# Performance work log

Measured on AMD Instinct MI355X. Metric: run time of the kernel, lower is better.

## Reference

```python
import jax, jax.numpy as jnp
import numpy as np

B, N, D = 2, 1024, 1024
H = 4
KD = 512          # key_dim = d_model * 0.5
VD = 1024         # value_dim = d_model
DK = KD // H      # 128 head_qk_dim
DV = VD // H      # 256 head_v_dim
LR = 16           # gate_low_rank_dim
GLN = 16.0        # gate_logit_normalizer
EPS = 1e-5


def setup_inputs() -> dict:
    key = jax.random.key(0)
    ks = jax.random.split(key, 10)
    s = 0.02
    return {
        "x": jax.random.normal(ks[0], (B, N, D), jnp.float32),
        "Wq": jax.random.normal(ks[1], (D, KD), jnp.float32) * s,
        "Wk": jax.random.normal(ks[2], (D, KD), jnp.float32) * s,
        "Wv": jax.random.normal(ks[3], (D, VD), jnp.float32) * s,
        "Wg": jax.random.normal(ks[4], (D, VD), jnp.float32) * s,
        "Wgk1": jax.random.normal(ks[5], (D, LR), jnp.float32) * s,
        "Wgk2": jax.random.normal(ks[6], (LR, KD), jnp.float32) * s,
        "bgk2": jax.random.normal(ks[7], (KD,), jnp.float32) * s,
        "Wout": jax.random.normal(ks[8], (VD, D), jnp.float32) * s,
        "rms_w": jnp.ones((DV,), jnp.float32),
    }


def _split_heads(t, h):
    b, n, hd = t.shape
    return t.reshape(b, n, h, hd // h).transpose(0, 2, 1, 3)  # b h n d


def _gla_scan(q, k, v, g):
    # q,k: [b,h,n,dk]; v: [b,h,n,dv]; g: [b,h,n,dk] (log-decay)
    b, h, n, dk = q.shape
    dv = v.shape[-1]
    qT = jnp.moveaxis(q, 2, 0)  # [n,b,h,dk]
    kT = jnp.moveaxis(k, 2, 0)
    vT = jnp.moveaxis(v, 2, 0)
    gT = jnp.moveaxis(g, 2, 0)

    def step(S, inp):
        qt, kt, vt, gt = inp
        # S_t = diag(exp(g_t)) S_{t-1} + k_t v_t^T ; o_t = q_t S_t
        S = S * jnp.exp(gt)[..., None] + kt[..., None] * vt[..., None, :]
        ot = jnp.einsum('bhk,bhkv->bhv', qt, S)
        return S, ot

    S0 = jnp.zeros((b, h, dk, dv), q.dtype)
    _, o = jax.lax.scan(step, S0, (qT, kT, vT, gT))
    return jnp.moveaxis(o, 0, 2)  # [b,h,n,dv]


def reference(x, Wq, Wk, Wv, Wg, Wgk1, Wgk2, bgk2, Wout, rms_w):
    q = _split_heads(x @ Wq, H)
    k = _split_heads(x @ Wk, H)
    v = _split_heads(x @ Wv, H)
    g = jax.nn.log_sigmoid((x @ Wgk1) @ Wgk2 + bgk2) / GLN
    g = jnp.maximum(g, -3.0)  # chunk mode clamp
    g = _split_heads(g, H)
    o = _gla_scan(q, k, v, g)               # [b,h,n,dv]
    o = o.transpose(0, 2, 1, 3)             # [b,n,h,dv]
    # RMSNorm over head_v_dim
    o = o * jax.lax.rsqrt(jnp.mean(o * o, axis=-1, keepdims=True) + EPS) * rms_w
    o = o.reshape(o.shape[0], o.shape[1], VD)
    o = o * jax.nn.silu(x @ Wg)
    return o @ Wout
```

## Files before the change

### kernel.cpp

```cpp
#include <hip/hip_runtime.h>
#include <math.h>


typedef __attribute__((ext_vector_type(4))) float vf4;
typedef __attribute__((ext_vector_type(4))) unsigned int vu4;
typedef __attribute__((ext_vector_type(8))) short short8;

#define DEVI static __device__ __forceinline__
DEVI vf4 vzero() { vf4 x = {0.f, 0.f, 0.f, 0.f}; return x; }

DEVI float bf2f(unsigned int u) {
  union { unsigned int i; float f; } c; c.i = u << 16; return c.f;
}
DEVI unsigned short f2bf(float f) {
  union { float f; unsigned int i; } c; c.f = f;
  unsigned int i = c.i;
  return (unsigned short)((i + 0x7fffu + ((i >> 16) & 1u)) >> 16);
}
DEVI void unpack8(vu4 r, float* f) {
  f[0] = bf2f(r.x & 0xffffu); f[1] = bf2f(r.x >> 16);
  f[2] = bf2f(r.y & 0xffffu); f[3] = bf2f(r.y >> 16);
  f[4] = bf2f(r.z & 0xffffu); f[5] = bf2f(r.z >> 16);
  f[6] = bf2f(r.w & 0xffffu); f[7] = bf2f(r.w >> 16);
}
DEVI void unpack16(const unsigned short* p, float* f) {
  unpack8(*(const vu4*)p, f);
  unpack8(*(const vu4*)(p + 8), f + 8);
}
DEVI vu4 pack8(const float* f) {
  vu4 o;
  o.x = (unsigned int)f2bf(f[0]) | ((unsigned int)f2bf(f[1]) << 16);
  o.y = (unsigned int)f2bf(f[2]) | ((unsigned int)f2bf(f[3]) << 16);
  o.z = (unsigned int)f2bf(f[4]) | ((unsigned int)f2bf(f[5]) << 16);
  o.w = (unsigned int)f2bf(f[6]) | ((unsigned int)f2bf(f[7]) << 16);
  return o;
}

__global__ __launch_bounds__(256)
void prep_k(const float* __restrict__ Wq, const float* __restrict__ Wk,
            const float* __restrict__ Wv, const float* __restrict__ Wg,
            const float* __restrict__ Wo, const float* __restrict__ X,
            unsigned short* __restrict__ wqT, unsigned short* __restrict__ wkT,
            unsigned short* __restrict__ wvT, unsigned short* __restrict__ wgT,
            unsigned short* __restrict__ woT, unsigned short* __restrict__ xb) {
  __shared__ float T[64][65];
  const int ct = blockIdx.x, kt = blockIdx.y;
  const int t = threadIdx.x;
  const int r = t >> 2, s = t & 3;
  if (ct >= 64) {
    const int rt = ct - 64;
    const size_t base = (size_t)(rt * 64 + r) * 1024 + kt * 64 + s * 16;
    float f[16];
    *(vf4*)&f[0]  = *(const vf4*)(X + base);
    *(vf4*)&f[4]  = *(const vf4*)(X + base + 4);
    *(vf4*)&f[8]  = *(const vf4*)(X + base + 8);
    *(vf4*)&f[12] = *(const vf4*)(X + base + 12);
    *(vu4*)(xb + base) = pack8(f);
    *(vu4*)(xb + base + 8) = pack8(f + 8);
    return;
  }
  const float* W; unsigned short* O; int N; int cb;
  if (ct < 8)       { W = Wq; O = wqT; N = 512;  cb = ct; }
  else if (ct < 16) { W = Wk; O = wkT; N = 512;  cb = ct - 8; }
  else if (ct < 32) { W = Wv; O = wvT; N = 1024; cb = ct - 16; }
  else if (ct < 48) { W = Wg; O = wgT; N = 1024; cb = ct - 32; }
  else              { W = Wo; O = woT; N = 1024; cb = ct - 48; }
  const float* src = W + (size_t)(kt * 64 + r) * N + cb * 64 + s * 16;
#pragma unroll
  for (int u = 0; u < 4; ++u) {
    vf4 v4 = *(const vf4*)(src + u * 4);
    T[r][s * 16 + u * 4 + 0] = v4.x;
    T[r][s * 16 + u * 4 + 1] = v4.y;
    T[r][s * 16 + u * 4 + 2] = v4.z;
    T[r][s * 16 + u * 4 + 3] = v4.w;
  }
  __syncthreads();
  unsigned int pk[8];
#pragma unroll
  for (int u = 0; u < 8; ++u) {
    unsigned int lo = f2bf(T[s * 16 + 2 * u][r]);
    unsigned int hi = f2bf(T[s * 16 + 2 * u + 1][r]);
    pk[u] = lo | (hi << 16);
  }
  unsigned short* dst = O + (size_t)(cb * 64 + r) * 1024 + kt * 64 + s * 16;
  *(vu4*)dst = *(vu4*)&pk[0];
  *(vu4*)(dst + 8) = *(vu4*)&pk[4];
}

__global__ __launch_bounds__(256)
void proj_mfma_k(const unsigned short* __restrict__ xb,
                 const unsigned short* __restrict__ wqT, const unsigned short* __restrict__ wkT,
                 const unsigned short* __restrict__ wvT, const unsigned short* __restrict__ wgT,
                 unsigned short* __restrict__ qb, unsigned short* __restrict__ kb,
                 unsigned short* __restrict__ vb, unsigned short* __restrict__ sgb) {
  __shared__ __align__(16) unsigned short As[128 * 72];
  __shared__ __align__(16) unsigned short Bs[128 * 72];
  const int t = threadIdx.x;
  const int m0 = blockIdx.y << 7;
  const int nt = blockIdx.x;
  const unsigned short* WT; int n0; int kind;
  if (nt < 4)       { WT = wqT; n0 = nt * 128;        kind = 0; }
  else if (nt < 8)  { WT = wkT; n0 = (nt - 4) * 128;  kind = 1; }
  else if (nt < 16) { WT = wvT; n0 = (nt - 8) * 128;  kind = 2; }
  else              { WT = wgT; n0 = (nt - 16) * 128; kind = 3; }

  const int w = t >> 6, lane = t & 63;
  const int wm = (w >> 1) * 64, wn = (w & 1) * 64;
  const int qd = lane >> 4, m = lane & 15;

  vf4 acc[4][4];
#pragma unroll
  for (int i = 0; i < 4; ++i)
#pragma unroll
    for (int j = 0; j < 4; ++j) acc[i][j] = vzero();

  for (int k0 = 0; k0 < 1024; k0 += 64) {
    __syncthreads();
#pragma unroll
    for (int u2 = 0; u2 < 4; ++u2) {
      const int id = t + (u2 << 8);
      const int row = id >> 3, kg = id & 7;
      vu4 ra = *(const vu4*)(xb + (size_t)(m0 + row) * 1024 + k0 + kg * 8);
      *(vu4*)&As[row * 72 + kg * 8] = ra;
      vu4 rb = *(const vu4*)(WT + (size_t)(n0 + row) * 1024 + k0 + kg * 8);
      *(vu4*)&Bs[row * 72 + kg * 8] = rb;
    }
    __syncthreads();
#pragma unroll
    for (int ks = 0; ks < 2; ++ks) {
      short8 af[4], bf[4];
#pragma unroll
      for (int i = 0; i < 4; ++i) {
        af[i] = *(const short8*)&As[(wm + i * 16 + m) * 72 + ks * 32 + qd * 8];
        bf[i] = *(const short8*)&Bs[(wn + i * 16 + m) * 72 + ks * 32 + qd * 8];
      }
#pragma unroll
      for (int i = 0; i < 4; ++i)
#pragma unroll
        for (int j = 0; j < 4; ++j)
          acc[i][j] = __builtin_amdgcn_mfma_f32_16x16x32_bf16(af[i], bf[j], acc[i][j], 0, 0, 0);
    }
  }
#pragma unroll
  for (int i = 0; i < 4; ++i) {
#pragma unroll
    for (int j = 0; j < 4; ++j) {
#pragma unroll
      for (int r = 0; r < 4; ++r) {
        const int grow = m0 + wm + i * 16 + qd * 4 + r;
        const int gcol = n0 + wn + j * 16 + m;
        float val = acc[i][j][r];
        if (kind == 0)      qb[(size_t)grow * 512 + gcol] = f2bf(val);
        else if (kind == 1) kb[(size_t)grow * 512 + gcol] = f2bf(val);
        else if (kind == 2) vb[(size_t)grow * 1024 + gcol] = f2bf(val);
        else {
          val = val / (1.f + expf(-val));
          sgb[(size_t)grow * 1024 + gcol] = f2bf(val);
        }
      }
    }
  }
}

__global__ __launch_bounds__(256)
void out_mfma_k(const unsigned short* __restrict__ Ab,
                const unsigned short* __restrict__ woT, float* __restrict__ Y) {
  __shared__ __align__(16) unsigned short As[128 * 72];
  __shared__ __align__(16) unsigned short Bs[128 * 72];
  const int t = threadIdx.x;
  const int m0 = blockIdx.y << 7;
  const int n0 = blockIdx.x << 7;
  const int w = t >> 6, lane = t & 63;
  const int wm = (w >> 1) * 64, wn = (w & 1) * 64;
  const int qd = lane >> 4, m = lane & 15;

  vf4 acc[4][4];
#pragma unroll
  for (int i = 0; i < 4; ++i)
#pragma unroll
    for (int j = 0; j < 4; ++j) acc[i][j] = vzero();

  for (int k0 = 0; k0 < 1024; k0 += 64) {
    __syncthreads();
#pragma unroll
    for (int u2 = 0; u2 < 4; ++u2) {
      const int id = t + (u2 << 8);
      const int row = id >> 3, kg = id & 7;
      vu4 ra = *(const vu4*)(Ab + (size_t)(m0 + row) * 1024 + k0 + kg * 8);
      *(vu4*)&As[row * 72 + kg * 8] = ra;
      vu4 rb = *(const vu4*)(woT + (size_t)(n0 + row) * 1024 + k0 + kg * 8);
      *(vu4*)&Bs[row * 72 + kg * 8] = rb;
    }
    __syncthreads();
#pragma unroll
    for (int ks = 0; ks < 2; ++ks) {
      short8 af[4], bf[4];
#pragma unroll
      for (int i = 0; i < 4; ++i) {
        af[i] = *(const short8*)&As[(wm + i * 16 + m) * 72 + ks * 32 + qd * 8];
        bf[i] = *(const short8*)&Bs[(wn + i * 16 + m) * 72 + ks * 32 + qd * 8];
      }
#pragma unroll
      for (int i = 0; i < 4; ++i)
#pragma unroll
        for (int j = 0; j < 4; ++j)
          acc[i][j] = __builtin_amdgcn_mfma_f32_16x16x32_bf16(af[i], bf[j], acc[i][j], 0, 0, 0);
    }
  }
#pragma unroll
  for (int i = 0; i < 4; ++i)
#pragma unroll
    for (int j = 0; j < 4; ++j)
#pragma unroll
      for (int r = 0; r < 4; ++r) {
        const int grow = m0 + wm + i * 16 + qd * 4 + r;
        const int gcol = n0 + wn + j * 16 + m;
        Y[(size_t)grow * 1024 + gcol] = acc[i][j][r];
      }
}

__global__ __launch_bounds__(64)
void lowrank_k(const float* __restrict__ X, const float* __restrict__ W1,
               float* __restrict__ xl) {
  const int row = blockIdx.x;
  const int t = threadIdx.x;
  float acc[16];
#pragma unroll
  for (int c2 = 0; c2 < 16; ++c2) acc[c2] = 0.f;
  const float* xp = X + (size_t)row * 1024 + t * 16;
  float xv[16];
#pragma unroll
  for (int u = 0; u < 4; ++u)
    *(vf4*)&xv[u * 4] = *(const vf4*)(xp + u * 4);
#pragma unroll
  for (int j = 0; j < 16; ++j) {
    const float* wp = W1 + (size_t)(t * 16 + j) * 16;
    float wv[16];
#pragma unroll
    for (int u = 0; u < 4; ++u)
      *(vf4*)&wv[u * 4] = *(const vf4*)(wp + u * 4);
#pragma unroll
    for (int c2 = 0; c2 < 16; ++c2) acc[c2] = fmaf(xv[j], wv[c2], acc[c2]);
  }
#pragma unroll
  for (int mm = 1; mm < 64; mm <<= 1) {
#pragma unroll
    for (int c2 = 0; c2 < 16; ++c2) acc[c2] += __shfl_xor(acc[c2], mm, 64);
  }
  if (t == 0) {
#pragma unroll
    for (int c2 = 0; c2 < 16; ++c2) xl[(size_t)row * 16 + c2] = acc[c2];
  }
}

__global__ __launch_bounds__(256)
void gate_scan_k(const float* __restrict__ xl, const float* __restrict__ W2,
                 const float* __restrict__ bias,
                 unsigned short* __restrict__ q, unsigned short* __restrict__ k,
                 float* __restrict__ ebtot) {
  const int t = threadIdx.x;
  const int w = t >> 6, lane = t & 63;
  const int wid = blockIdx.x * 4 + w;
  const int kcol = wid & 511;
  const int c = (wid >> 9) & 15;
  const int b = wid >> 13;
  const size_t rowbase = (size_t)b * 1024 + c * 64;

  const float* xp = xl + (rowbase + lane) * 16;
  float xv[16];
#pragma unroll
  for (int u = 0; u < 4; ++u)
    *(vf4*)&xv[u * 4] = *(const vf4*)(xp + u * 4);
  float z = bias[kcol];
#pragma unroll
  for (int r = 0; r < 16; ++r) z = fmaf(xv[r], W2[r * 512 + kcol], z);
  float ls = fminf(z, 0.f) - log1pf(expf(-fabsf(z)));
  float g = fmaxf(ls * (1.f / 16.f), -3.f);

#pragma unroll
  for (int d = 1; d < 64; d <<= 1) {
    float up = __shfl_up(g, d, 64);
    if (lane >= d) g += up;
  }

  const size_t a = (rowbase + lane) * 512 + kcol;
  float qv = bf2f((unsigned int)q[a]) * expf(g);
  float kv = bf2f((unsigned int)k[a]) * expf(fminf(-g, 80.f));
  q[a] = f2bf(qv);
  k[a] = f2bf(kv);
  if (lane == 63)
    ebtot[((size_t)b * 16 + c) * 512 + kcol] = expf(g);
}

__global__ __launch_bounds__(256)
void intra_k(const unsigned short* __restrict__ q16, const unsigned short* __restrict__ k16,
             const unsigned short* __restrict__ v, float* __restrict__ o) {
  __shared__ __align__(16) unsigned short Qs[64 * 136];
  __shared__ __align__(16) unsigned short Ks[64 * 136];
  __shared__ float As[64 * 68];
  __shared__ float Vs[64 * 64];
  const int t = threadIdx.x;
  const int vh = blockIdx.x, c = blockIdx.y, bh = blockIdx.z;
  const int b = bh >> 2, h = bh & 3;
  const size_t rowbase = (size_t)b * 1024 + c * 64;

#pragma unroll
  for (int u2 = 0; u2 < 4; ++u2) {
    const int id = t + (u2 << 8);
    const int row = id >> 4, kg = id & 15;
    *(vu4*)&Qs[row * 136 + kg * 8] =
        *(const vu4*)(q16 + (rowbase + row) * 512 + h * 128 + kg * 8);
    *(vu4*)&Ks[row * 136 + kg * 8] =
        *(const vu4*)(k16 + (rowbase + row) * 512 + h * 128 + kg * 8);
  }
  __syncthreads();

  {
    const int w = t >> 6, lane = t & 63;
    const int qd = lane >> 4, m = lane & 15;
    short8 af[4];
#pragma unroll
    for (int kf = 0; kf < 4; ++kf)
      af[kf] = *(const short8*)&Qs[(w * 16 + m) * 136 + kf * 32 + qd * 8];
    vf4 acc[4];
#pragma unroll
    for (int jt = 0; jt < 4; ++jt) acc[jt] = vzero();
#pragma unroll
    for (int jt = 0; jt < 4; ++jt)
#pragma unroll
      for (int kf = 0; kf < 4; ++kf) {
        short8 bfr = *(const short8*)&Ks[(jt * 16 + m) * 136 + kf * 32 + qd * 8];
        acc[jt] = __builtin_amdgcn_mfma_f32_16x16x32_bf16(af[kf], bfr, acc[jt], 0, 0, 0);
      }
#pragma unroll
    for (int jt = 0; jt < 4; ++jt)
#pragma unroll
      for (int r = 0; r < 4; ++r) {
        const int i = w * 16 + qd * 4 + r;
        const int j = jt * 16 + m;
        As[i * 68 + j] = (j <= i) ? acc[jt][r] : 0.f;
      }
  }

  const int i2 = t >> 2, sb = t & 3;
  for (int p = 0; p < 2; ++p) {
    const int vt = vh * 2 + p;
    __syncthreads();
    {
      const int r = t >> 2, s = t & 3;
      const unsigned short* vp = v + (rowbase + r) * 1024 + h * 256 + vt * 64 + s * 16;
      float f[16];
      unpack16(vp, f);
#pragma unroll
      for (int u = 0; u < 16; ++u) Vs[r * 64 + s * 16 + u] = f[u];
    }
    __syncthreads();
    vf4 acc[4];
#pragma unroll
    for (int u = 0; u < 4; ++u) acc[u] = vzero();
    for (int jj = 0; jj < 64; ++jj) {
      const float a = As[i2 * 68 + jj];
#pragma unroll
      for (int u = 0; u < 4; ++u)
        acc[u] += a * *(const vf4*)&Vs[jj * 64 + sb * 16 + u * 4];
    }
    float* op = o + (rowbase + i2) * 1024 + h * 256 + vt * 64 + sb * 16;
#pragma unroll
    for (int u = 0; u < 4; ++u) *(vf4*)(op + u * 4) = acc[u];
  }
}

__global__ __launch_bounds__(256)
void kv_k(const unsigned short* __restrict__ k16, const unsigned short* __restrict__ v,
          unsigned short* __restrict__ ST) {
  __shared__ float Ks[64 * 128];
  __shared__ float Vs[64 * 64];
  const int t = threadIdx.x;
  const int vt = blockIdx.x, c = blockIdx.y, bh = blockIdx.z;
  const int b = bh >> 2, h = bh & 3;
  const size_t rowbase = (size_t)b * 1024 + c * 64;
  {
    const int r = t >> 2, s = t & 3;
    const unsigned short* kp = k16 + (rowbase + r) * 512 + h * 128 + s * 32;
    float fk[32];
    unpack16(kp, fk);
    unpack16(kp + 16, fk + 16);
#pragma unroll
    for (int u = 0; u < 8; ++u)
      *(vf4*)&Ks[r * 128 + s * 32 + u * 4] = *(const vf4*)&fk[u * 4];
    const unsigned short* vp = v + (rowbase + r) * 1024 + h * 256 + vt * 64 + s * 16;
    float f[16];
    unpack16(vp, f);
#pragma unroll
    for (int u = 0; u < 16; ++u) Vs[r * 64 + s * 16 + u] = f[u];
  }
  __syncthreads();
  const int kk = t >> 1, half = t & 1;
  float su[32];
#pragma unroll
  for (int u = 0; u < 32; ++u) su[u] = 0.f;
  for (int j = 0; j < 64; ++j) {
    const float kv = Ks[j * 128 + kk];
    const float* vrow = &Vs[j * 64 + half * 32];
#pragma unroll
    for (int u = 0; u < 32; ++u) su[u] = fmaf(kv, vrow[u], su[u]);
  }
  unsigned short* Sp = ST + ((size_t)(bh * 16 + c) * 256 + vt * 64 + half * 32) * 128 + kk;
#pragma unroll
  for (int u = 0; u < 32; ++u)
    Sp[(size_t)u * 128] = f2bf(su[u]);
}

__global__ __launch_bounds__(256)
void state_scan_k(unsigned short* __restrict__ ST, const float* __restrict__ ebtot) {
  const int idx = blockIdx.x * 256 + threadIdx.x;
  const int kg = idx & 15;
  const int vv = (idx >> 4) & 255;
  const int bh = idx >> 12;
  const int b = bh >> 2, h = bh & 3;
  float s[8];
#pragma unroll
  for (int u = 0; u < 8; ++u) s[u] = 0.f;
  for (int c = 0; c < 16; ++c) {
    unsigned short* p = ST + ((size_t)(bh * 16 + c) * 256 + vv) * 128 + kg * 8;
    const float* ep = ebtot + ((size_t)b * 16 + c) * 512 + h * 128 + kg * 8;
    float e[8];
    *(vf4*)&e[0] = *(const vf4*)ep;
    *(vf4*)&e[4] = *(const vf4*)(ep + 4);
    float kv[8];
    unpack8(*(const vu4*)p, kv);
    *(vu4*)p = pack8(s);
#pragma unroll
    for (int u = 0; u < 8; ++u) s[u] = (s[u] + kv[u]) * e[u];
  }
}

__global__ __launch_bounds__(256)
void o_inter_k(const unsigned short* __restrict__ q16, const unsigned short* __restrict__ ST,
               float* __restrict__ o) {
  __shared__ __align__(16) unsigned short Qs[64 * 136];
  __shared__ __align__(16) unsigned short Ss[128 * 136];
  const int t = threadIdx.x;
  const int vt = blockIdx.x, c = blockIdx.y, bh = blockIdx.z;
  const int b = bh >> 2, h = bh & 3;
  const size_t rowbase = (size_t)b * 1024 + c * 64;

#pragma unroll
  for (int u2 = 0; u2 < 4; ++u2) {
    const int id = t + (u2 << 8);
    const int row = id >> 4, kg = id & 15;
    *(vu4*)&Qs[row * 136 + kg * 8] =
        *(const vu4*)(q16 + (rowbase + row) * 512 + h * 128 + kg * 8);
  }
#pragma unroll
  for (int u2 = 0; u2 < 8; ++u2) {
    const int id = t + (u2 << 8);
    const int vrow = id >> 4, kg = id & 15;
    *(vu4*)&Ss[vrow * 136 + kg * 8] =
        *(const vu4*)(ST + ((size_t)(bh * 16 + c) * 256 + vt * 128 + vrow) * 128 + kg * 8);
  }
  __syncthreads();

  const int w = t >> 6, lane = t & 63;
  const int qd = lane >> 4, m = lane & 15;
  short8 af[4];
#pragma unroll
  for (int kf = 0; kf < 4; ++kf)
    af[kf] = *(const short8*)&Qs[(w * 16 + m) * 136 + kf * 32 + qd * 8];
#pragma unroll
  for (int nt = 0; nt < 8; ++nt) {
    vf4 acc = vzero();
#pragma unroll
    for (int kf = 0; kf < 4; ++kf) {
      short8 bfr = *(const short8*)&Ss[(nt * 16 + m) * 136 + kf * 32 + qd * 8];
      acc = __builtin_amdgcn_mfma_f32_16x16x32_bf16(af[kf], bfr, acc, 0, 0, 0);
    }
    float* base = o + (rowbase + w * 16 + qd * 4) * 1024 + h * 256 + vt * 128 + nt * 16 + m;
#pragma unroll
    for (int r = 0; r < 4; ++r)
      base[(size_t)r * 1024] += acc[r];
  }
}

__global__ __launch_bounds__(256)
void norm_gate_k(const float* __restrict__ o, const float* __restrict__ rmsw,
                 const unsigned short* __restrict__ sg,
                 unsigned short* __restrict__ ob) {
  __shared__ float red[4];
  const int grp = blockIdx.x;
  const int row = grp >> 2, h = grp & 3;
  const int t = threadIdx.x;
  const size_t idx = (size_t)row * 1024 + h * 256 + t;
  const float val = o[idx];
  float ss = val * val;
#pragma unroll
  for (int mm = 1; mm < 64; mm <<= 1) ss += __shfl_xor(ss, mm, 64);
  if ((t & 63) == 0) red[t >> 6] = ss;
  __syncthreads();
  const float tot = red[0] + red[1] + red[2] + red[3];
  const float scale = rsqrtf(tot * (1.f / 256.f) + 1e-5f);
  ob[idx] = f2bf(val * scale * rmsw[t] * bf2f((unsigned int)sg[idx]));
}

extern "C" void kernel_launch(void* const* d_in, const int* in_sizes, int n_in,
                              void* d_out, int out_size, void* d_ws, size_t ws_size,
                              hipStream_t stream) {
  const float* x    = (const float*)d_in[0];
  const float* Wq   = (const float*)d_in[1];
  const float* Wk   = (const float*)d_in[2];
  const float* Wv   = (const float*)d_in[3];
  const float* Wg   = (const float*)d_in[4];
  const float* Wgk1 = (const float*)d_in[5];
  const float* Wgk2 = (const float*)d_in[6];
  const float* bgk2 = (const float*)d_in[7];
  const float* Wout = (const float*)d_in[8];
  const float* rmsw = (const float*)d_in[9];

  const size_t MB = 1u << 20;
  char* w = (char*)d_ws;
  unsigned short* qb16   = (unsigned short*)(w);
  unsigned short* kb16   = (unsigned short*)(w + 2 * MB);
  unsigned short* vbuf   = (unsigned short*)(w + 4 * MB);
  unsigned short* sgbuf  = (unsigned short*)(w + 8 * MB);
  float*          obuf   = (float*)(w + 12 * MB);
  char*           sreg   = w + 20 * MB;
  unsigned short* xb     = (unsigned short*)sreg;
  unsigned short* STbuf  = (unsigned short*)sreg;
  unsigned short* obuf_b = (unsigned short*)sreg;
  float*          xlbuf  = (float*)(w + 28 * MB);
  float*          ebbuf  = (float*)(w + 28 * MB + 131072);
  unsigned short* wqT    = (unsigned short*)(w + 29 * MB);
  unsigned short* wkT    = (unsigned short*)(w + 30 * MB);
  unsigned short* wvT    = (unsigned short*)(w + 31 * MB);
  unsigned short* wgT    = (unsigned short*)(w + 33 * MB);
  unsigned short* woT    = (unsigned short*)(w + 35 * MB);

  prep_k<<<dim3(96, 16), 256, 0, stream>>>(Wq, Wk, Wv, Wg, Wout, x,
                                           wqT, wkT, wvT, wgT, woT, xb);
  lowrank_k<<<2048, 64, 0, stream>>>(x, Wgk1, xlbuf);
  proj_mfma_k<<<dim3(24, 16), 256, 0, stream>>>(xb, wqT, wkT, wvT, wgT, qb16, kb16, vbuf, sgbuf);
  gate_scan_k<<<4096, 256, 0, stream>>>(xlbuf, Wgk2, bgk2, qb16, kb16, ebbuf);
  intra_k<<<dim3(2, 16, 8), 256, 0, stream>>>(qb16, kb16, vbuf, obuf);
  kv_k<<<dim3(4, 16, 8), 256, 0, stream>>>(kb16, vbuf, STbuf);
  state_scan_k<<<128, 256, 0, stream>>>(STbuf, ebbuf);
  o_inter_k<<<dim3(2, 16, 8), 256, 0, stream>>>(qb16, STbuf, obuf);
  norm_gate_k<<<8192, 256, 0, stream>>>(obuf, rmsw, sgbuf, obuf_b);
  out_mfma_k<<<dim3(8, 16), 256, 0, stream>>>(obuf_b, woT, (float*)d_out);
}
```

Before: 226.3 us.

## Fuse intra-chunk attention and chunk state computation into one MFMA kernel

Merges the intra-chunk attention kernel and the per-chunk K^T V state kernel into one kernel that loads Q, K and V once into shared memory. Transposed K and V tiles are kept in LDS. Both the A·V product and the K^T V state product now use bf16 MFMA instructions instead of scalar fp32 FMA loops. This removes a kernel launch and the duplicate global loads of K and V. In exchange, the attention matrix A is rounded to bf16 before multiplying V, and the scattered transposed LDS writes may cause bank conflicts.

```diff
diff --git a/kernel.cpp b/kernel.cpp
--- a/kernel.cpp
+++ b/kernel.cpp
@@ -22,10 +22,6 @@
   f[2] = bf2f(r.y & 0xffffu); f[3] = bf2f(r.y >> 16);
   f[4] = bf2f(r.z & 0xffffu); f[5] = bf2f(r.z >> 16);
   f[6] = bf2f(r.w & 0xffffu); f[7] = bf2f(r.w >> 16);
-}
-DEVI void unpack16(const unsigned short* p, float* f) {
-  unpack8(*(const vu4*)p, f);
-  unpack8(*(const vu4*)(p + 8), f + 8);
 }
 DEVI vu4 pack8(const float* f) {
   vu4 o;
@@ -293,12 +289,14 @@
 }
 
 __global__ __launch_bounds__(256)
-void intra_k(const unsigned short* __restrict__ q16, const unsigned short* __restrict__ k16,
-             const unsigned short* __restrict__ v, float* __restrict__ o) {
+void intra_kv_k(const unsigned short* __restrict__ q16, const unsigned short* __restrict__ k16,
+                const unsigned short* __restrict__ v, float* __restrict__ o,
+                unsigned short* __restrict__ ST) {
   __shared__ __align__(16) unsigned short Qs[64 * 136];
   __shared__ __align__(16) unsigned short Ks[64 * 136];
-  __shared__ float As[64 * 68];
-  __shared__ float Vs[64 * 64];
+  __shared__ __align__(16) unsigned short Kt[128 * 68];
+  __shared__ __align__(16) unsigned short Vt[128 * 68];
+  __shared__ __align__(16) unsigned short Asb[64 * 68];
   const int t = threadIdx.x;
   const int vh = blockIdx.x, c = blockIdx.y, bh = blockIdx.z;
   const int b = bh >> 2, h = bh & 3;
@@ -308,16 +306,26 @@
   for (int u2 = 0; u2 < 4; ++u2) {
     const int id = t + (u2 << 8);
     const int row = id >> 4, kg = id & 15;
-    *(vu4*)&Qs[row * 136 + kg * 8] =
-        *(const vu4*)(q16 + (rowbase + row) * 512 + h * 128 + kg * 8);
-    *(vu4*)&Ks[row * 136 + kg * 8] =
-        *(const vu4*)(k16 + (rowbase + row) * 512 + h * 128 + kg * 8);
+    vu4 rq = *(const vu4*)(q16 + (rowbase + row) * 512 + h * 128 + kg * 8);
+    *(vu4*)&Qs[row * 136 + kg * 8] = rq;
+    vu4 rk = *(const vu4*)(k16 + (rowbase + row) * 512 + h * 128 + kg * 8);
+    *(vu4*)&Ks[row * 136 + kg * 8] = rk;
+    const unsigned short* kp = (const unsigned short*)&rk;
+#pragma unroll
+    for (int u = 0; u < 8; ++u)
+      Kt[(kg * 8 + u) * 68 + row] = kp[u];
+    vu4 rv = *(const vu4*)(v + (rowbase + row) * 1024 + h * 256 + vh * 128 + kg * 8);
+    const unsigned short* vp = (const unsigned short*)&rv;
+#pragma unroll
+    for (int u = 0; u < 8; ++u)
+      Vt[(kg * 8 + u) * 68 + row] = vp[u];
   }
   __syncthreads();
 
+  const int w = t >> 6, lane = t & 63;
+  const int qd = lane >> 4, m = lane & 15;
+
   {
-    const int w = t >> 6, lane = t & 63;
-    const int qd = lane >> 4, m = lane & 15;
     short8 af[4];
 #pragma unroll
     for (int kf = 0; kf < 4; ++kf)
@@ -338,77 +346,62 @@
       for (int r = 0; r < 4; ++r) {
         const int i = w * 16 + qd * 4 + r;
         const int j = jt * 16 + m;
-        As[i * 68 + j] = (j <= i) ? acc[jt][r] : 0.f;
-      }
-  }
-
-  const int i2 = t >> 2, sb = t & 3;
-  for (int p = 0; p < 2; ++p) {
-    const int vt = vh * 2 + p;
-    __syncthreads();
-    {
-      const int r = t >> 2, s = t & 3;
-      const unsigned short* vp = v + (rowbase + r) * 1024 + h * 256 + vt * 64 + s * 16;
-      float f[16];
-      unpack16(vp, f);
-#pragma unroll
-      for (int u = 0; u < 16; ++u) Vs[r * 64 + s * 16 + u] = f[u];
-    }
-    __syncthreads();
-    vf4 acc[4];
-#pragma unroll
-    for (int u = 0; u < 4; ++u) acc[u] = vzero();
-    for (int jj = 0; jj < 64; ++jj) {
-      const float a = As[i2 * 68 + jj];
-#pragma unroll
-      for (int u = 0; u < 4; ++u)
-        acc[u] += a * *(const vf4*)&Vs[jj * 64 + sb * 16 + u * 4];
-    }
-    float* op = o + (rowbase + i2) * 1024 + h * 256 + vt * 64 + sb * 16;
-#pragma unroll
-    for (int u = 0; u < 4; ++u) *(vf4*)(op + u * 4) = acc[u];
-  }
-}
-
-__global__ __launch_bounds__(256)
-void kv_k(const unsigned short* __restrict__ k16, const unsigned short* __restrict__ v,
-          unsigned short* __restrict__ ST) {
-  __shared__ float Ks[64 * 128];
-  __shared__ float Vs[64 * 64];
-  const int t = threadIdx.x;
-  const int vt = blockIdx.x, c = blockIdx.y, bh = blockIdx.z;
-  const int b = bh >> 2, h = bh & 3;
-  const size_t rowbase = (size_t)b * 1024 + c * 64;
+        Asb[i * 68 + j] = f2bf((j <= i) ? acc[jt][r] : 0.f);
+      }
+  }
+  __syncthreads();
+
   {
-    const int r = t >> 2, s = t & 3;
-    const unsigned short* kp = k16 + (rowbase + r) * 512 + h * 128 + s * 32;
-    float fk[32];
-    unpack16(kp, fk);
-    unpack16(kp + 16, fk + 16);
-#pragma unroll
-    for (int u = 0; u < 8; ++u)
-      *(vf4*)&Ks[r * 128 + s * 32 + u * 4] = *(const vf4*)&fk[u * 4];
-    const unsigned short* vp = v + (rowbase + r) * 1024 + h * 256 + vt * 64 + s * 16;
-    float f[16];
-    unpack16(vp, f);
-#pragma unroll
-    for (int u = 0; u < 16; ++u) Vs[r * 64 + s * 16 + u] = f[u];
-  }
-  __syncthreads();
-  const int kk = t >> 1, half = t & 1;
-  float su[32];
-#pragma unroll
-  for (int u = 0; u < 32; ++u) su[u] = 0.f;
-  for (int j = 0; j < 64; ++j) {
-    const float kv = Ks[j * 128 + kk];
-    const float* vrow = &Vs[j * 64 + half * 32];
-#pragma unroll
-    for (int u = 0; u < 32; ++u) su[u] = fmaf(kv, vrow[u], su[u]);
-  }
-  unsigned short* Sp = ST + ((size_t)(bh * 16 + c) * 256 + vt * 64 + half * 32) * 128 + kk;
-#pragma unroll
-  for (int u = 0; u < 32; ++u)
-    Sp[(size_t)u * 128] = f2bf(su[u]);
+    vf4 acc2[4][2];
+#pragma unroll
+    for (int mt = 0; mt < 4; ++mt) { acc2[mt][0] = vzero(); acc2[mt][1] = vzero(); }
+#pragma unroll
+    for (int kf = 0; kf < 2; ++kf) {
+      short8 bf0 = *(const short8*)&Vt[(w * 32 + m) * 68 + kf * 32 + qd * 8];
+      short8 bf1 = *(const short8*)&Vt[(w * 32 + 16 + m) * 68 + kf * 32 + qd * 8];
+#pragma unroll
+      for (int mt = 0; mt < 4; ++mt) {
+        short8 af = *(const short8*)&Asb[(mt * 16 + m) * 68 + kf * 32 + qd * 8];
+        acc2[mt][0] = __builtin_amdgcn_mfma_f32_16x16x32_bf16(af, bf0, acc2[mt][0], 0, 0, 0);
+        acc2[mt][1] = __builtin_amdgcn_mfma_f32_16x16x32_bf16(af, bf1, acc2[mt][1], 0, 0, 0);
+      }
+    }
+#pragma unroll
+    for (int mt = 0; mt < 4; ++mt)
+#pragma unroll
+      for (int nt = 0; nt < 2; ++nt)
+#pragma unroll
+        for (int r = 0; r < 4; ++r) {
+          const int i = mt * 16 + qd * 4 + r;
+          const int vc = h * 256 + vh * 128 + w * 32 + nt * 16 + m;
+          o[(rowbase + i) * 1024 + vc] = acc2[mt][nt][r];
+        }
+  }
+
+  {
+    short8 af3[2][2];
+#pragma unroll
+    for (int mt = 0; mt < 2; ++mt)
+#pragma unroll
+      for (int kf = 0; kf < 2; ++kf)
+        af3[mt][kf] = *(const short8*)&Vt[(w * 32 + mt * 16 + m) * 68 + kf * 32 + qd * 8];
+#pragma unroll
+    for (int nt = 0; nt < 8; ++nt) {
+      vf4 a0 = vzero(), a1 = vzero();
+#pragma unroll
+      for (int kf = 0; kf < 2; ++kf) {
+        short8 bfr = *(const short8*)&Kt[(nt * 16 + m) * 68 + kf * 32 + qd * 8];
+        a0 = __builtin_amdgcn_mfma_f32_16x16x32_bf16(af3[0][kf], bfr, a0, 0, 0, 0);
+        a1 = __builtin_amdgcn_mfma_f32_16x16x32_bf16(af3[1][kf], bfr, a1, 0, 0, 0);
+      }
+      const size_t sbase = (size_t)(bh * 16 + c) * 256 + vh * 128 + w * 32;
+#pragma unroll
+      for (int r = 0; r < 4; ++r) {
+        ST[(sbase + qd * 4 + r) * 128 + nt * 16 + m] = f2bf(a0[r]);
+        ST[(sbase + 16 + qd * 4 + r) * 128 + nt * 16 + m] = f2bf(a1[r]);
+      }
+    }
+  }
 }
 
 __global__ __launch_bounds__(256)
@@ -540,8 +533,7 @@
   lowrank_k<<<2048, 64, 0, stream>>>(x, Wgk1, xlbuf);
   proj_mfma_k<<<dim3(24, 16), 256, 0, stream>>>(xb, wqT, wkT, wvT, wgT, qb16, kb16, vbuf, sgbuf);
   gate_scan_k<<<4096, 256, 0, stream>>>(xlbuf, Wgk2, bgk2, qb16, kb16, ebbuf);
-  intra_k<<<dim3(2, 16, 8), 256, 0, stream>>>(qb16, kb16, vbuf, obuf);
-  kv_k<<<dim3(4, 16, 8), 256, 0, stream>>>(kb16, vbuf, STbuf);
+  intra_kv_k<<<dim3(2, 16, 8), 256, 0, stream>>>(qb16, kb16, vbuf, obuf, STbuf);
   state_scan_k<<<128, 256, 0, stream>>>(STbuf, ebbuf);
   o_inter_k<<<dim3(2, 16, 8), 256, 0, stream>>>(qb16, STbuf, obuf);
   norm_gate_k<<<8192, 256, 0, stream>>>(obuf, rmsw, sgbuf, obuf_b);
```

Measured after the change: 209.3 us. 7.5% less time.
